# Kernel optimization log

Measured on AMD Instinct MI355X. Metric: run time of the kernel, lower is better.

## Reference

```python
import jax, jax.numpy as jnp
import numpy as np

B, S, W, D, T = 64, 512, 384, 768, 21


def setup_inputs() -> dict:
    key = jax.random.key(0)
    ks = jax.random.split(key, 8)
    hidden_states = jax.random.normal(ks[0], (B, S, D), dtype=jnp.float32)  # BERT last_hidden_state
    word_maps = jnp.sort(jax.random.randint(ks[1], (B, W), 0, S), axis=1)  # first-subword index per word
    tags = jax.random.randint(ks[2], (B, W), 0, T)
    word_mask = jnp.ones((B, W), dtype=bool)  # torchcrf requires mask[:,0] all on
    W_tag = jax.random.normal(ks[3], (T, D), dtype=jnp.float32) * 0.02  # hidden2tag weight
    b_tag = jnp.zeros((T,), dtype=jnp.float32)
    start_trans = jax.random.uniform(ks[4], (T,), minval=-0.1, maxval=0.1)
    end_trans = jax.random.uniform(ks[5], (T,), minval=-0.1, maxval=0.1)
    trans = jax.random.uniform(ks[6], (T, T), minval=-0.1, maxval=0.1)
    return dict(hidden_states=hidden_states, W_tag=W_tag, b_tag=b_tag,
                start_trans=start_trans, end_trans=end_trans, trans=trans,
                word_maps=word_maps, tags=tags, word_mask=word_mask)


def reference(hidden_states, W_tag, b_tag, start_trans, end_trans, trans,
              word_maps, tags, word_mask):
    # --- ragged subword -> word gather (vectorized form of the python loop) ---
    word_feats = jnp.take_along_axis(hidden_states, word_maps[:, :, None], axis=1)  # [B,W,D]
    # dropout is identity in eval / deterministic reference
    emissions = jnp.einsum('bwd,td->bwt', word_feats, W_tag) + b_tag  # [B,W,T]

    maskf = word_mask.astype(emissions.dtype)
    bidx = jnp.arange(tags.shape[0])

    # --- CRF numerator: score of the given tag sequence ---
    emit_sc = jnp.take_along_axis(emissions, tags[:, :, None], axis=2)[..., 0]  # [B,W]
    trans_sc = trans[tags[:, :-1], tags[:, 1:]]                                  # [B,W-1]
    num = start_trans[tags[:, 0]] + emit_sc[:, 0]
    num = num + jnp.sum((trans_sc + emit_sc[:, 1:]) * maskf[:, 1:], axis=1)
    lengths = word_mask.sum(axis=1)
    last_tags = jnp.take_along_axis(tags, (lengths - 1)[:, None], axis=1)[:, 0]
    num = num + end_trans[last_tags]

    # --- CRF denominator: log partition via forward recurrence (scan over time) ---
    def step(score, xm):
        em_t, m_t = xm  # [B,T], [B]
        nxt = jax.nn.logsumexp(score[:, :, None] + trans[None, :, :] + em_t[:, None, :], axis=1)
        return jnp.where(m_t[:, None], nxt, score), None

    score0 = start_trans[None, :] + emissions[:, 0]  # [B,T]
    score, _ = jax.lax.scan(step, score0,
                            (jnp.swapaxes(emissions[:, 1:], 0, 1), word_mask[:, 1:].T))
    log_z = jax.nn.logsumexp(score + end_trans[None, :], axis=1)  # [B]

    llh = num - log_z
    return -jnp.mean(llh)  # reduction='mean', negated
```

## Files before the change

### kernel.cpp

```cpp
#include <hip/hip_runtime.h>
#include <math.h>

#define BB 64
#define SS 512
#define WW 384
#define DD 768
#define TT 21
#define ROWS (BB*WW)
#define EMSTRIDE (WW*TT)

__global__ __launch_bounds__(256) void emissions_kernel(
    const float* __restrict__ hidden, const int* __restrict__ word_maps,
    const float* __restrict__ W_tag, const float* __restrict__ b_tag,
    float* __restrict__ em, float* __restrict__ out)
{
    __shared__ __align__(16) float feat[64 * 68];
    __shared__ __align__(16) float wtag[TT * 68];
    __shared__ int rowoff[64];

    const int tid = threadIdx.x;
    const int rowBase = blockIdx.x * 64;

    if (blockIdx.x == 0 && tid == 0) out[0] = 0.0f;

    if (tid < 64) {
        int row = rowBase + tid;
        int b = row / WW;
        int w = row - b * WW;
        rowoff[tid] = b * SS + word_maps[b * WW + w];
    }
    __syncthreads();

    const int rgrp = tid >> 2;
    const int tg   = tid & 3;

    float acc[6];
    #pragma unroll
    for (int j = 0; j < 6; ++j) acc[j] = 0.0f;

    const int r0 = tid >> 4;
    const int q  = tid & 15;

    for (int c = 0; c < DD / 64; ++c) {
        for (int i = tid; i < TT * 16; i += 256) {
            int t = i >> 4, qq = i & 15;
            *(float4*)&wtag[t * 68 + qq * 4] =
                *(const float4*)&W_tag[t * DD + c * 64 + qq * 4];
        }
        #pragma unroll
        for (int p = 0; p < 4; ++p) {
            int r = p * 16 + r0;
            *(float4*)&feat[r * 68 + q * 4] =
                *(const float4*)&hidden[(size_t)rowoff[r] * DD + c * 64 + q * 4];
        }
        __syncthreads();

        #pragma unroll 4
        for (int d4 = 0; d4 < 16; ++d4) {
            float4 fa = *(const float4*)&feat[rgrp * 68 + d4 * 4];
            #pragma unroll
            for (int j = 0; j < 6; ++j) {
                int t = tg + 4 * j;
                if (t < TT) {
                    float4 wv = *(const float4*)&wtag[t * 68 + d4 * 4];
                    acc[j] = fmaf(fa.x, wv.x, fmaf(fa.y, wv.y,
                             fmaf(fa.z, wv.z, fmaf(fa.w, wv.w, acc[j]))));
                }
            }
        }
        __syncthreads();
    }

    const int rowA = rowBase + rgrp;
    #pragma unroll
    for (int j = 0; j < 6; ++j) {
        int t = tg + 4 * j;
        if (t < TT) {
            em[(size_t)rowA * TT + t] = acc[j] + b_tag[t];
        }
    }
}

__device__ __forceinline__ float lane_bcast(float v, int l) {
    return __uint_as_float(__builtin_amdgcn_readlane(__float_as_uint(v), l));
}

__global__ __launch_bounds__(256) void crf_kernel(
    const float* __restrict__ em, const int* __restrict__ tags,
    const float* __restrict__ start_trans, const float* __restrict__ end_trans,
    const float* __restrict__ trans, float* __restrict__ out)
{
    __shared__ __align__(16) float sem[(WW + 2) * TT];

    const int b = blockIdx.x;
    const int tid = threadIdx.x;
    const float* emb = em + (size_t)b * EMSTRIDE;

    for (int i = tid; i < EMSTRIDE / 4; i += 256)
        ((float4*)sem)[i] = ((const float4*)emb)[i];
    for (int i = tid; i < 2 * TT; i += 256) sem[EMSTRIDE + i] = 0.0f;
    __syncthreads();

    if (tid >= 64) return;

    const int j = tid;
    const int jj = (j < TT) ? j : (TT - 1);

    float E[TT];
    #pragma unroll
    for (int i = 0; i < TT; ++i) E[i] = __expf(trans[i * TT + jj]);

    float s = start_trans[jj] + sem[jj];

    float em1 = sem[1 * TT + jj];
    float em2 = sem[2 * TT + jj];
    for (int t = 1; t < WW; ++t) {
        float em_cur = em1;
        em1 = em2;
        em2 = sem[(t + 2) * TT + jj];
        float M = lane_bcast(s, 0);
        float p = __expf(s - M);
        float a0 = 0.f, a1 = 0.f, a2 = 0.f;
        #pragma unroll
        for (int i = 0; i < TT; i += 3) {
            a0 = fmaf(lane_bcast(p, i    ), E[i    ], a0);
            a1 = fmaf(lane_bcast(p, i + 1), E[i + 1], a1);
            a2 = fmaf(lane_bcast(p, i + 2), E[i + 2], a2);
        }
        s = em_cur + M + __logf(a0 + a1 + a2);
    }

    float v = (j < TT) ? (s + end_trans[jj]) : -1e30f;
    float m = v;
    #pragma unroll
    for (int o = 32; o > 0; o >>= 1) m = fmaxf(m, __shfl_xor(m, o));
    float pe = (j < TT) ? __expf(v - m) : 0.0f;
    float ssum = pe;
    #pragma unroll
    for (int o = 32; o > 0; o >>= 1) ssum += __shfl_xor(ssum, o);
    float lz = m + __logf(ssum);

    const int* tb = tags + b * WW;
    float part = 0.f;
    for (int w = j; w < WW; w += 64) {
        int tw = tb[w];
        float e = sem[w * TT + tw];
        float tsc = (w == 0) ? start_trans[tw] : trans[tb[w - 1] * TT + tw];
        part += tsc + e;
    }
    #pragma unroll
    for (int o = 32; o > 0; o >>= 1) part += __shfl_xor(part, o);

    if (j == 0) {
        float num = part + end_trans[tb[WW - 1]];
        atomicAdd(out, -(num - lz) * (1.0f / BB));
    }
}

extern "C" void kernel_launch(void* const* d_in, const int* in_sizes, int n_in,
                              void* d_out, int out_size, void* d_ws, size_t ws_size,
                              hipStream_t stream) {
    const float* hidden      = (const float*)d_in[0];
    const float* W_tag       = (const float*)d_in[1];
    const float* b_tag       = (const float*)d_in[2];
    const float* start_trans = (const float*)d_in[3];
    const float* end_trans   = (const float*)d_in[4];
    const float* trans       = (const float*)d_in[5];
    const int*   word_maps   = (const int*)  d_in[6];
    const int*   tags        = (const int*)  d_in[7];

    float* out = (float*)d_out;
    float* em  = (float*)d_ws;

    emissions_kernel<<<ROWS / 64, 256, 0, stream>>>(hidden, word_maps, W_tag, b_tag, em, out);
    crf_kernel<<<BB, 256, 0, stream>>>(em, tags, start_trans, end_trans, trans, out);
}
```

Measured before the change: 240.8 us.

## Parallelize CRF forward recurrence via chunked transfer-matrix products

```diff
diff --git a/kernel.cpp b/kernel.cpp
--- a/kernel.cpp
+++ b/kernel.cpp
@@ -8,6 +8,11 @@
 #define TT 21
 #define ROWS (BB*WW)
 #define EMSTRIDE (WW*TT)
+#define NCH 16
+#define CLEN 24
+#define PSTRIDE 24
+#define PMATSZ (TT*PSTRIDE)
+#define LN32 3.4657359027997265f
 
 __global__ __launch_bounds__(256) void emissions_kernel(
     const float* __restrict__ hidden, const int* __restrict__ word_maps,
@@ -15,7 +20,6 @@
     float* __restrict__ em, float* __restrict__ out)
 {
     __shared__ __align__(16) float feat[64 * 68];
-    __shared__ __align__(16) float wtag[TT * 68];
     __shared__ int rowoff[64];
 
     const int tid = threadIdx.x;
@@ -42,11 +46,6 @@
     const int q  = tid & 15;
 
     for (int c = 0; c < DD / 64; ++c) {
-        for (int i = tid; i < TT * 16; i += 256) {
-            int t = i >> 4, qq = i & 15;
-            *(float4*)&wtag[t * 68 + qq * 4] =
-                *(const float4*)&W_tag[t * DD + c * 64 + qq * 4];
-        }
         #pragma unroll
         for (int p = 0; p < 4; ++p) {
             int r = p * 16 + r0;
@@ -62,7 +61,7 @@
             for (int j = 0; j < 6; ++j) {
                 int t = tg + 4 * j;
                 if (t < TT) {
-                    float4 wv = *(const float4*)&wtag[t * 68 + d4 * 4];
+                    float4 wv = *(const float4*)&W_tag[(size_t)t * DD + c * 64 + d4 * 4];
                     acc[j] = fmaf(fa.x, wv.x, fmaf(fa.y, wv.y,
                              fmaf(fa.z, wv.z, fmaf(fa.w, wv.w, acc[j]))));
                 }
@@ -75,76 +74,166 @@
     #pragma unroll
     for (int j = 0; j < 6; ++j) {
         int t = tg + 4 * j;
-        if (t < TT) {
-            em[(size_t)rowA * TT + t] = acc[j] + b_tag[t];
-        }
-    }
+        if (t < TT) em[(size_t)rowA * TT + t] = acc[j] + b_tag[t];
+    }
+}
+
+__global__ __launch_bounds__(256) void chunk_kernel(
+    const float* __restrict__ em, const float* __restrict__ trans,
+    float* __restrict__ Pmat)
+{
+    __shared__ __align__(16) float Pbuf[4][2][PMATSZ];
+    __shared__ __align__(16) float gem[4][CLEN * PSTRIDE];
+
+    const int wid  = threadIdx.x >> 6;
+    const int lane = threadIdx.x & 63;
+    const int id   = blockIdx.x * 4 + wid;
+    const int b    = id >> 4;
+    const int c    = id & (NCH - 1);
+    const int s0   = 1 + c * CLEN;
+    const int n    = (c == NCH - 1) ? (WW - s0) : CLEN;
+
+    int i3r = lane / 6;
+    const int jg  = lane - i3r * 6;
+    const bool active = (i3r < 7) && (jg < 6);
+    const int i3 = (i3r < 7) ? i3r : 6;
+    const int jbase = (jg < 6 ? jg : 5) * 4;
+
+    float4 etr[CLEN];
+    #pragma unroll
+    for (int k = 0; k < CLEN; ++k) {
+        float4 e = make_float4(0.f, 0.f, 0.f, 0.f);
+        if (k < TT) {
+            e.x = (jbase + 0 < TT) ? __expf(trans[k * TT + jbase + 0]) * 0.03125f : 0.f;
+            e.y = (jbase + 1 < TT) ? __expf(trans[k * TT + jbase + 1]) * 0.03125f : 0.f;
+            e.z = (jbase + 2 < TT) ? __expf(trans[k * TT + jbase + 2]) * 0.03125f : 0.f;
+            e.w = (jbase + 3 < TT) ? __expf(trans[k * TT + jbase + 3]) * 0.03125f : 0.f;
+        }
+        etr[k] = e;
+    }
+
+    for (int idx = lane; idx < n * PSTRIDE; idx += 64) {
+        int tt = idx / PSTRIDE, j = idx - tt * PSTRIDE;
+        float g = 1.0f;
+        if (j < TT) g = __expf(em[((size_t)b * WW + (s0 + tt)) * TT + j]);
+        gem[wid][idx] = g;
+    }
+
+    {
+        float4 g = *(const float4*)&gem[wid][0 * PSTRIDE + jbase];
+        #pragma unroll
+        for (int r = 0; r < 3; ++r) {
+            int i = i3 * 3 + r;
+            float4 e = etr[i];
+            float4 v = make_float4(e.x * g.x, e.y * g.y, e.z * g.z, e.w * g.w);
+            if (active) *(float4*)&Pbuf[wid][0][i * PSTRIDE + jbase] = v;
+        }
+    }
+    __syncthreads();
+
+    int pp = 0;
+    for (int tt = 1; tt < n; ++tt) {
+        float acc[3][4];
+        #pragma unroll
+        for (int r = 0; r < 3; ++r)
+            #pragma unroll
+            for (int q = 0; q < 4; ++q) acc[r][q] = 0.f;
+
+        const float* Pc = &Pbuf[wid][pp][0];
+        #pragma unroll
+        for (int kb = 0; kb < 6; ++kb) {
+            float4 p0 = *(const float4*)&Pc[(i3 * 3 + 0) * PSTRIDE + kb * 4];
+            float4 p1 = *(const float4*)&Pc[(i3 * 3 + 1) * PSTRIDE + kb * 4];
+            float4 p2 = *(const float4*)&Pc[(i3 * 3 + 2) * PSTRIDE + kb * 4];
+            #pragma unroll
+            for (int kk = 0; kk < 4; ++kk) {
+                float4 e = etr[kb * 4 + kk];
+                float a = (kk == 0) ? p0.x : (kk == 1) ? p0.y : (kk == 2) ? p0.z : p0.w;
+                float bv= (kk == 0) ? p1.x : (kk == 1) ? p1.y : (kk == 2) ? p1.z : p1.w;
+                float cv= (kk == 0) ? p2.x : (kk == 1) ? p2.y : (kk == 2) ? p2.z : p2.w;
+                acc[0][0] = fmaf(a, e.x, acc[0][0]); acc[0][1] = fmaf(a, e.y, acc[0][1]);
+                acc[0][2] = fmaf(a, e.z, acc[0][2]); acc[0][3] = fmaf(a, e.w, acc[0][3]);
+                acc[1][0] = fmaf(bv, e.x, acc[1][0]); acc[1][1] = fmaf(bv, e.y, acc[1][1]);
+                acc[1][2] = fmaf(bv, e.z, acc[1][2]); acc[1][3] = fmaf(bv, e.w, acc[1][3]);
+                acc[2][0] = fmaf(cv, e.x, acc[2][0]); acc[2][1] = fmaf(cv, e.y, acc[2][1]);
+                acc[2][2] = fmaf(cv, e.z, acc[2][2]); acc[2][3] = fmaf(cv, e.w, acc[2][3]);
+            }
+        }
+        float4 g = *(const float4*)&gem[wid][tt * PSTRIDE + jbase];
+        if (active) {
+            #pragma unroll
+            for (int r = 0; r < 3; ++r) {
+                float4 v = make_float4(acc[r][0] * g.x, acc[r][1] * g.y,
+                                       acc[r][2] * g.z, acc[r][3] * g.w);
+                *(float4*)&Pbuf[wid][1 - pp][(i3 * 3 + r) * PSTRIDE + jbase] = v;
+            }
+        }
+        pp ^= 1;
+    }
+
+    float* dst = Pmat + (size_t)id * PMATSZ;
+    for (int idx = lane; idx < PMATSZ; idx += 64)
+        dst[idx] = Pbuf[wid][pp][idx];
 }
 
 __device__ __forceinline__ float lane_bcast(float v, int l) {
     return __uint_as_float(__builtin_amdgcn_readlane(__float_as_uint(v), l));
 }
 
-__global__ __launch_bounds__(256) void crf_kernel(
-    const float* __restrict__ em, const int* __restrict__ tags,
-    const float* __restrict__ start_trans, const float* __restrict__ end_trans,
-    const float* __restrict__ trans, float* __restrict__ out)
+__global__ __launch_bounds__(64) void combine_kernel(
+    const float* __restrict__ Pmat, const float* __restrict__ em,
+    const int* __restrict__ tags, const float* __restrict__ start_trans,
+    const float* __restrict__ end_trans, const float* __restrict__ trans,
+    float* __restrict__ out)
 {
-    __shared__ __align__(16) float sem[(WW + 2) * TT];
-
     const int b = blockIdx.x;
-    const int tid = threadIdx.x;
+    const int j = threadIdx.x;
+    const bool act = (j < TT);
+    const int jc = act ? j : (TT - 1);
     const float* emb = em + (size_t)b * EMSTRIDE;
 
-    for (int i = tid; i < EMSTRIDE / 4; i += 256)
-        ((float4*)sem)[i] = ((const float4*)emb)[i];
-    for (int i = tid; i < 2 * TT; i += 256) sem[EMSTRIDE + i] = 0.0f;
-    __syncthreads();
-
-    if (tid >= 64) return;
-
-    const int j = tid;
-    const int jj = (j < TT) ? j : (TT - 1);
-
-    float E[TT];
-    #pragma unroll
-    for (int i = 0; i < TT; ++i) E[i] = __expf(trans[i * TT + jj]);
-
-    float s = start_trans[jj] + sem[jj];
-
-    float em1 = sem[1 * TT + jj];
-    float em2 = sem[2 * TT + jj];
-    for (int t = 1; t < WW; ++t) {
-        float em_cur = em1;
-        em1 = em2;
-        em2 = sem[(t + 2) * TT + jj];
-        float M = lane_bcast(s, 0);
-        float p = __expf(s - M);
+    float s0v = start_trans[jc] + emb[jc];
+    float M = act ? s0v : -1e30f;
+    #pragma unroll
+    for (int o = 32; o > 0; o >>= 1) M = fmaxf(M, __shfl_xor(M, o));
+    float sig = act ? __expf(s0v - M) : 0.0f;
+
+    for (int c = 0; c < NCH; ++c) {
+        const float* P = Pmat + (size_t)(b * NCH + c) * PMATSZ;
+        float col[TT];
+        #pragma unroll
+        for (int i = 0; i < TT; ++i) col[i] = P[i * PSTRIDE + jc];
         float a0 = 0.f, a1 = 0.f, a2 = 0.f;
         #pragma unroll
         for (int i = 0; i < TT; i += 3) {
-            a0 = fmaf(lane_bcast(p, i    ), E[i    ], a0);
-            a1 = fmaf(lane_bcast(p, i + 1), E[i + 1], a1);
-            a2 = fmaf(lane_bcast(p, i + 2), E[i + 2], a2);
-        }
-        s = em_cur + M + __logf(a0 + a1 + a2);
-    }
-
-    float v = (j < TT) ? (s + end_trans[jj]) : -1e30f;
-    float m = v;
-    #pragma unroll
-    for (int o = 32; o > 0; o >>= 1) m = fmaxf(m, __shfl_xor(m, o));
-    float pe = (j < TT) ? __expf(v - m) : 0.0f;
+            a0 = fmaf(lane_bcast(sig, i    ), col[i    ], a0);
+            a1 = fmaf(lane_bcast(sig, i + 1), col[i + 1], a1);
+            a2 = fmaf(lane_bcast(sig, i + 2), col[i + 2], a2);
+        }
+        float v = act ? (a0 + a1 + a2) : 0.0f;
+        float m = v;
+        #pragma unroll
+        for (int o = 32; o > 0; o >>= 1) m = fmaxf(m, __shfl_xor(m, o));
+        int nst = (c == NCH - 1) ? (WW - (1 + c * CLEN)) : CLEN;
+        M += __logf(m) + (float)nst * LN32;
+        sig = v / m;
+    }
+
+    float fin = (act && sig > 0.f) ? (M + __logf(sig) + end_trans[jc]) : -1e30f;
+    float mm = fin;
+    #pragma unroll
+    for (int o = 32; o > 0; o >>= 1) mm = fmaxf(mm, __shfl_xor(mm, o));
+    float pe = __expf(fin - mm);
     float ssum = pe;
     #pragma unroll
     for (int o = 32; o > 0; o >>= 1) ssum += __shfl_xor(ssum, o);
-    float lz = m + __logf(ssum);
+    float lz = mm + __logf(ssum);
 
     const int* tb = tags + b * WW;
     float part = 0.f;
     for (int w = j; w < WW; w += 64) {
         int tw = tb[w];
-        float e = sem[w * TT + tw];
+        float e = emb[w * TT + tw];
         float tsc = (w == 0) ? start_trans[tw] : trans[tb[w - 1] * TT + tw];
         part += tsc + e;
     }
@@ -169,9 +258,11 @@
     const int*   word_maps   = (const int*)  d_in[6];
     const int*   tags        = (const int*)  d_in[7];
 
-    float* out = (float*)d_out;
-    float* em  = (float*)d_ws;
+    float* out  = (float*)d_out;
+    float* em   = (float*)d_ws;
+    float* Pmat = (float*)d_ws + (size_t)ROWS * TT;
 
     emissions_kernel<<<ROWS / 64, 256, 0, stream>>>(hidden, word_maps, W_tag, b_tag, em, out);
-    crf_kernel<<<BB, 256, 0, stream>>>(em, tags, start_trans, end_trans, trans, out);
-}
+    chunk_kernel<<<BB * NCH / 4, 256, 0, stream>>>(em, trans, Pmat);
+    combine_kernel<<<BB, 64, 0, stream>>>(Pmat, em, tags, start_trans, end_trans, trans, out);
+}
```

Result: slower. 404.1 us (+67.8%).
